# Performance work log

Hardware: AMD Instinct MI355X
Metric: run time of the kernel (lower is better)

## Reference

```python
import jax, jax.numpy as jnp
import numpy as np

D_MODEL, D_K, D_V, H, N, B = 512, 64, 64, 8, 2048, 2


def _xavier(key, shape):
    fan_out, fan_in = shape
    a = jnp.sqrt(6.0 / (fan_in + fan_out))
    return jax.random.uniform(key, shape, jnp.float32, -a, a)


def setup_inputs() -> dict:
    key = jax.random.key(0)
    ks = jax.random.split(key, 12)
    inp = {
        "regions_out": jax.random.normal(ks[0], (B, N, D_MODEL), jnp.float32),
        "grids_out": jax.random.normal(ks[1], (B, N, D_MODEL), jnp.float32),
        "interests": jax.random.normal(ks[2], (B, N, D_MODEL), jnp.float32),
        "attention_mask_regions": jax.random.randint(ks[3], (B, 1, 1, N), 0, 2, jnp.int32),
        "attention_mask_grids": jax.random.randint(ks[4], (B, 1, 1, N), 0, 2, jnp.int32),
        "attention_weights": jax.random.uniform(ks[5], (B, 1, 1, N), jnp.float32),
        # nn.Linear params (weight [out,in], bias [out]); xavier_uniform weights, zero bias
        "Wq": _xavier(ks[6], (H * D_K, D_MODEL)), "bq": jnp.zeros((H * D_K,), jnp.float32),
        "Wk": _xavier(ks[7], (H * D_K, D_MODEL)), "bk": jnp.zeros((H * D_K,), jnp.float32),
        "Wv": _xavier(ks[8], (H * D_V, D_MODEL)), "bv": jnp.zeros((H * D_V,), jnp.float32),
        "Wq12": _xavier(ks[9], (H * D_K, D_MODEL)), "bq12": jnp.zeros((H * D_K,), jnp.float32),
        "Wo1": _xavier(ks[10], (D_MODEL, H * D_V)), "bo1": jnp.zeros((D_MODEL,), jnp.float32),
        "Wo2": _xavier(ks[11], (D_MODEL, H * D_V)), "bo2": jnp.zeros((D_MODEL,), jnp.float32),
    }
    return inp


def _proj(x, W, b, d):
    # x: [b, n, d_model] -> [b, h, n, d]
    b_s, n, _ = x.shape
    y = x @ W.T + b
    return y.reshape(b_s, n, H, d).transpose(0, 2, 1, 3)


def reference(regions_out, grids_out, interests, attention_mask_regions,
              attention_mask_grids, attention_weights,
              Wq, bq, Wk, bk, Wv, bv, Wq12, bq12, Wo1, bo1, Wo2, bo2):
    b_s, nq, _ = interests.shape
    scale = 1.0 / np.sqrt(D_K).astype(np.float32)

    q = _proj(interests, Wq, bq, D_K)          # [b,h,nq,dk]
    q1 = _proj(regions_out, Wq12, bq12, D_K)   # [b,h,nk1,dk]
    q2 = _proj(grids_out, Wq12, bq12, D_K)     # [b,h,nk1,dk]
    k1 = _proj(regions_out, Wk, bk, D_K)       # [b,h,nk1,dk]
    k2 = _proj(grids_out, Wk, bk, D_K)
    v1 = _proj(regions_out, Wv, bv, D_V)
    v2 = _proj(grids_out, Wv, bv, D_V)

    att1 = jnp.einsum("bhqd,bhkd->bhqk", q + q2, k1) * scale
    att2 = jnp.einsum("bhqd,bhkd->bhqk", q + q1, k2) * scale
    att1 = att1 * attention_weights
    att2 = att2 * attention_weights
    att1 = jnp.where(attention_mask_regions.astype(bool), -jnp.inf, att1)
    att2 = jnp.where(attention_mask_grids.astype(bool), -jnp.inf, att2)
    att1 = jax.nn.softmax(att1, axis=-1)
    att2 = jax.nn.softmax(att2, axis=-1)
    # dropout is identity in eval mode

    out1 = jnp.einsum("bhqk,bhkd->bhqd", att1, v1).transpose(0, 2, 1, 3).reshape(b_s, nq, H * D_V)
    out2 = jnp.einsum("bhqk,bhkd->bhqd", att2, v2).transpose(0, 2, 1, 3).reshape(b_s, nq, H * D_V)
    out1 = out1 @ Wo1.T + bo1
    out2 = out2 @ Wo2.T + bo2
    return (out1, out2)
```

## Files before the change

kernel.cpp:

```cpp
#include <hip/hip_runtime.h>
#include <hip/hip_bf16.h>

typedef __attribute__((ext_vector_type(8))) __bf16 bf16x8;
typedef __attribute__((ext_vector_type(4))) float f32x4;
typedef __attribute__((ext_vector_type(4))) int   i32x4;
typedef unsigned short u16;

#define WS_SEG 2097152

static __device__ __forceinline__ u16 f2b(float f) {
  __hip_bfloat16 h = __float2bfloat16(f);
  return __builtin_bit_cast(u16, h);
}
static __device__ __forceinline__ i32x4 cvt8(const float* __restrict__ p) {
  float4 a = *(const float4*)p;
  float4 b = *(const float4*)(p + 4);
  union { i32x4 v; u16 u[8]; } r;
  r.u[0]=f2b(a.x); r.u[1]=f2b(a.y); r.u[2]=f2b(a.z); r.u[3]=f2b(a.w);
  r.u[4]=f2b(b.x); r.u[5]=f2b(b.y); r.u[6]=f2b(b.z); r.u[7]=f2b(b.w);
  return r.v;
}
static __device__ __forceinline__ float fexp2(float x) {
  float r; asm("v_exp_f32 %0, %1" : "=v"(r) : "v"(x)); return r;
}
template<int C>
static __device__ __forceinline__ float dppf(float x) {
  int v = __builtin_amdgcn_update_dpp(__builtin_bit_cast(int, x),
                                      __builtin_bit_cast(int, x), C, 0xF, 0xF, false);
  return __builtin_bit_cast(float, v);
}
static __device__ __forceinline__ float rowsum16(float x) {
  x += dppf<0xB1>(x);
  x += dppf<0x4E>(x);
  x += dppf<0x141>(x);
  x += dppf<0x140>(x);
  return x;
}
static __device__ __forceinline__ void gld16(const u16* gp, u16* lp) {
  __builtin_amdgcn_global_load_lds(
      (const __attribute__((address_space(1))) void*)gp,
      (__attribute__((address_space(3))) void*)lp, 16, 0, 0);
}

__global__ __launch_bounds__(256) void convert_kernel(
    const float* __restrict__ regions, const float* __restrict__ grids,
    const float* __restrict__ interests,
    const float* __restrict__ Wq, const float* __restrict__ Wk,
    const float* __restrict__ Wv, const float* __restrict__ Wq12,
    const float* __restrict__ Wo1, const float* __restrict__ Wo2,
    u16* __restrict__ ws)
{
  const size_t i = (size_t)(blockIdx.x * 256 + threadIdx.x) * 8;
  const float* s; u16* d;
  if (i < 2097152)      { s = regions   + i;           d = ws + 6 * WS_SEG + i; }
  else if (i < 4194304) { s = grids     + (i - 2097152); d = ws + 7 * WS_SEG + (i - 2097152); }
  else if (i < 6291456) { s = interests + (i - 4194304); d = ws + 8 * WS_SEG + (i - 4194304); }
  else {
    const size_t j = i - 6291456;
    d = ws + 9 * WS_SEG + j;
    if (j < 262144)       s = Wq  + j;
    else if (j < 524288)  s = Wk  + (j - 262144);
    else if (j < 786432)  s = Wv  + (j - 524288);
    else if (j < 1048576) s = Wq12+ (j - 786432);
    else if (j < 1310720) s = Wo1 + (j - 1048576);
    else                  s = Wo2 + (j - 1310720);
  }
  *(i32x4*)d = cvt8(s);
}

template<int MT>
__global__ __launch_bounds__(256, 2) void gemm_all(
    const float* __restrict__ aw,
    const float* __restrict__ bq,  const float* __restrict__ bk,
    const float* __restrict__ bv,  const float* __restrict__ bq12,
    const float* __restrict__ bo1, const float* __restrict__ bo2,
    u16* __restrict__ ws, float* __restrict__ out, int phase)
{
  __shared__ u16 As[MT * 64];
  __shared__ u16 Bs[128 * 64];
  constexpr int MFR = MT / 32;

  const u16* regs_bf = ws + 6 * WS_SEG;
  const u16* grid_bf = ws + 7 * WS_SEG;
  const u16* intr_bf = ws + 8 * WS_SEG;
  const u16* Wt      = ws + 9 * WS_SEG;

  const u16 *A1 = nullptr, *A2 = nullptr, *B1 = nullptr, *B2 = nullptr;
  const float *bias1 = nullptr, *bias2 = nullptr;
  u16* dst16 = nullptr;
  float* dst32 = nullptr;
  int KT = 512, epi = 0;
  const int z = blockIdx.z;
  if (phase == 0) {
    if (z == 0)      { A1=intr_bf; A2=grid_bf; B1=Wt; B2=Wt+786432; KT=1024; bias1=bq; bias2=bq12; epi=0; dst16=ws+0*WS_SEG; }
    else if (z == 1) { A1=intr_bf; A2=regs_bf; B1=Wt; B2=Wt+786432; KT=1024; bias1=bq; bias2=bq12; epi=0; dst16=ws+1*WS_SEG; }
    else if (z == 2) { A1=regs_bf; B1=Wt+262144; bias1=bk; epi=1; dst16=ws+2*WS_SEG; }
    else if (z == 3) { A1=grid_bf; B1=Wt+262144; bias1=bk; epi=1; dst16=ws+3*WS_SEG; }
    else if (z == 4) { A1=regs_bf; B1=Wt+524288; bias1=bv; epi=3; dst16=ws+4*WS_SEG; }
    else             { A1=grid_bf; B1=Wt+524288; bias1=bv; epi=3; dst16=ws+5*WS_SEG; }
  } else {
    if (z == 0) { A1=ws+6*WS_SEG; B1=Wt+1048576; bias1=bo1; epi=2; dst32=out; }
    else        { A1=ws+7*WS_SEG; B1=Wt+1310720; bias1=bo2; epi=2; dst32=out + 2097152; }
  }
  const bool swp = (epi == 3);

  const int t = threadIdx.x;
  const int lane = t & 63, w = t >> 6;
  const int l15 = lane & 15, q4 = lane >> 4;
  const int m0 = blockIdx.y * MT, j0 = blockIdx.x * 128;
  const int ro = (w >> 1) * (MT / 2), co = (w & 1) * 64;

  f32x4 acc[MFR][4];
  for (int i = 0; i < MFR; i++)
    for (int j = 0; j < 4; j++) acc[i][j] = (f32x4){0.f, 0.f, 0.f, 0.f};

  for (int k0 = 0; k0 < KT; k0 += 64) {
    const u16* pa; const u16* pb; int kk = k0, ra, rb;
    if (swp)           { pa = B1; pb = A1; ra = j0; rb = m0; }
    else if (kk < 512) { pa = A1; pb = B1; ra = m0; rb = j0; }
    else               { pa = A2; pb = B2; ra = m0; rb = j0; kk -= 512; }
    __syncthreads();
#pragma unroll
    for (int c = 0; c < MFR; c++) {
      const int cidx = w * MFR + c;
      const int row = cidx * 8 + (lane >> 3);
      const int cg = (lane & 7) ^ (row & 7);
      gld16(&pa[(ra + row) * 512 + kk + cg * 8], &As[cidx * 512]);
    }
#pragma unroll
    for (int c = 0; c < 4; c++) {
      const int cidx = w * 4 + c;
      const int row = cidx * 8 + (lane >> 3);
      const int cg = (lane & 7) ^ (row & 7);
      gld16(&pb[(rb + row) * 512 + kk + cg * 8], &Bs[cidx * 512]);
    }
    __syncthreads();
#pragma unroll
    for (int h = 0; h < 2; h++) {
      bf16x8 af[MFR], bfr[4];
#pragma unroll
      for (int i = 0; i < MFR; i++) {
        const int r = ro + i * 16 + l15;
        af[i] = *(const bf16x8*)&As[r * 64 + (((h * 4 + q4) ^ (r & 7)) * 8)];
      }
#pragma unroll
      for (int i = 0; i < 4; i++) {
        const int r = co + i * 16 + l15;
        bfr[i] = *(const bf16x8*)&Bs[r * 64 + (((h * 4 + q4) ^ (r & 7)) * 8)];
      }
#pragma unroll
      for (int mt = 0; mt < MFR; mt++)
#pragma unroll
        for (int nt = 0; nt < 4; nt++)
          acc[mt][nt] = __builtin_amdgcn_mfma_f32_16x16x32_bf16(af[mt], bfr[nt], acc[mt][nt], 0, 0, 0);
    }
  }

  if (epi == 2) {
#pragma unroll
    for (int nt = 0; nt < 4; nt++) {
      const int j = j0 + co + nt * 16 + l15;
      const float bsum = bias1[j];
#pragma unroll
      for (int mt = 0; mt < MFR; mt++)
#pragma unroll
        for (int r = 0; r < 4; r++) {
          const int m = m0 + ro + mt * 16 + q4 * 4 + r;
          dst32[m * 512 + j] = acc[mt][nt][r] + bsum;
        }
    }
    return;
  }

  __syncthreads();
  u16* Es = ((w < 2) ? As : Bs) + (w & 1) * 4096;

  if (epi == 3) {
#pragma unroll
    for (int mt = 0; mt < MFR; mt++)
#pragma unroll
      for (int r = 0; r < 4; r++) {
        const int rr = mt * 16 + q4 * 4 + r;
        const float bias = bias1[j0 + ro + rr];
#pragma unroll
        for (int nt = 0; nt < 4; nt++)
          Es[rr * 64 + (((nt * 2 + (l15 >> 3)) ^ (rr & 7)) * 8) + (l15 & 7)] =
              f2b(acc[mt][nt][r] + bias);
      }
  } else {
    float bsum4[4];
#pragma unroll
    for (int nt = 0; nt < 4; nt++) {
      const int j = j0 + co + nt * 16 + l15;
      bsum4[nt] = bias1[j] + (bias2 ? bias2[j] : 0.f);
    }
#pragma unroll
    for (int mt = 0; mt < MFR; mt++)
#pragma unroll
      for (int r = 0; r < 4; r++) {
        const int rr = mt * 16 + q4 * 4 + r;
        const float awm = (epi == 1) ? 0.18033688f * aw[m0 + ro + rr] : 1.f;
#pragma unroll
        for (int nt = 0; nt < 4; nt++)
          Es[rr * 64 + (((nt * 2 + (l15 >> 3)) ^ (rr & 7)) * 8) + (l15 & 7)] =
              f2b((acc[mt][nt][r] + bsum4[nt]) * awm);
      }
  }
  asm volatile("s_waitcnt lgkmcnt(0)" ::: "memory");

#pragma unroll
  for (int g = 0; g < 8; g++) {
    const int rr2 = g * 8 + (lane >> 3);
    i32x4 val = *(const i32x4*)&Es[rr2 * 64 + (((lane & 7) ^ (rr2 & 7)) * 8)];
    if (epi == 3) {
      const int hd = j0 + ro + rr2;
      const int token0 = m0 + co;
      *(i32x4*)&dst16[((size_t)(token0 >> 11) * 512 + hd) * 2048 + (token0 & 2047) + (lane & 7) * 8] = val;
    } else {
      const int tk = m0 + ro + rr2;
      *(i32x4*)&dst16[(size_t)tk * 512 + j0 + co + (lane & 7) * 8] = val;
    }
  }
}

__global__ __launch_bounds__(256, 2) void attn_kernel(
    const int* __restrict__ mask_r, const int* __restrict__ mask_g,
    u16* __restrict__ ws)
{
  const int qt = blockIdx.x, bh = blockIdx.y, path = blockIdx.z;
  const int b = bh >> 3, h = bh & 7;
  const u16* Q  = (path ? ws + 1 * WS_SEG : ws + 0 * WS_SEG) + (size_t)(b * 2048 + qt * 128) * 512 + h * 64;
  const u16* K  = (path ? ws + 3 * WS_SEG : ws + 2 * WS_SEG) + (size_t)(b * 2048) * 512 + h * 64;
  const u16* Vg = (path ? ws + 5 * WS_SEG : ws + 4 * WS_SEG) + (size_t)(b * 512 + h * 64) * 2048;
  const int* mask = (path ? mask_g : mask_r) + b * 2048;
  u16* O = (path ? ws + 7 * WS_SEG : ws + 6 * WS_SEG) + (size_t)(b * 2048 + qt * 128) * 512 + h * 64;

  __shared__ u16 Ks[64 * 64];
  __shared__ u16 Vs[64 * 64];
  __shared__ u16 Ps[128 * 64];
  __shared__ float Ms[2048];

  const int t = threadIdx.x, lane = t & 63, w = t >> 6;
  const int l15 = lane & 15, q4 = lane >> 4;

  {
    const int4 a = *(const int4*)&mask[t * 8];
    const int4 c = *(const int4*)&mask[t * 8 + 4];
    float4 f1, f2v;
    f1.x = (a.x ? -1e30f : 0.f) - 16.f; f1.y = (a.y ? -1e30f : 0.f) - 16.f;
    f1.z = (a.z ? -1e30f : 0.f) - 16.f; f1.w = (a.w ? -1e30f : 0.f) - 16.f;
    f2v.x = (c.x ? -1e30f : 0.f) - 16.f; f2v.y = (c.y ? -1e30f : 0.f) - 16.f;
    f2v.z = (c.z ? -1e30f : 0.f) - 16.f; f2v.w = (c.w ? -1e30f : 0.f) - 16.f;
    *(float4*)&Ms[t * 8] = f1;
    *(float4*)&Ms[t * 8 + 4] = f2v;
  }

  bf16x8 qf[2][2];
#pragma unroll
  for (int mt = 0; mt < 2; mt++) {
    const int qrow = w * 32 + mt * 16 + l15;
    qf[mt][0] = *(const bf16x8*)&Q[qrow * 512 + q4 * 8];
    qf[mt][1] = *(const bf16x8*)&Q[qrow * 512 + 32 + q4 * 8];
  }

  float l_run[2][4];
  f32x4 o_acc[2][4];
#pragma unroll
  for (int mt = 0; mt < 2; mt++) {
#pragma unroll
    for (int r = 0; r < 4; r++) l_run[mt][r] = 0.f;
#pragma unroll
    for (int d = 0; d < 4; d++) o_acc[mt][d] = (f32x4){0.f, 0.f, 0.f, 0.f};
  }

  for (int kt = 0; kt < 32; kt++) {
    __syncthreads();
#pragma unroll
    for (int c = 0; c < 2; c++) {
      const int cidx = w * 2 + c;
      const int row = cidx * 8 + (lane >> 3);
      const int cg = (lane & 7) ^ (row & 7);
      gld16(&K[(size_t)(kt * 64 + row) * 512 + cg * 8], &Ks[cidx * 512]);
      gld16(&Vg[row * 2048 + kt * 64 + cg * 8], &Vs[cidx * 512]);
    }
    __syncthreads();

    f32x4 s[2][4];
#pragma unroll
    for (int mt = 0; mt < 2; mt++)
#pragma unroll
      for (int nt = 0; nt < 4; nt++) s[mt][nt] = (f32x4){0.f, 0.f, 0.f, 0.f};
#pragma unroll
    for (int nt = 0; nt < 4; nt++)
#pragma unroll
      for (int ss = 0; ss < 2; ss++) {
        const int r = nt * 16 + l15;
        bf16x8 kf = *(const bf16x8*)&Ks[r * 64 + (((ss * 4 + q4) ^ (r & 7)) * 8)];
        s[0][nt] = __builtin_amdgcn_mfma_f32_16x16x32_bf16(qf[0][ss], kf, s[0][nt], 0, 0, 0);
        s[1][nt] = __builtin_amdgcn_mfma_f32_16x16x32_bf16(qf[1][ss], kf, s[1][nt], 0, 0, 0);
      }

#pragma unroll
    for (int nt = 0; nt < 4; nt++) {
      const float bias = Ms[kt * 64 + nt * 16 + l15];
#pragma unroll
      for (int mt = 0; mt < 2; mt++)
#pragma unroll
        for (int r = 0; r < 4; r++) {
          const float p = fexp2(s[mt][nt][r] + bias);
          s[mt][nt][r] = p;
          l_run[mt][r] += p;
        }
    }

#pragma unroll
    for (int mt = 0; mt < 2; mt++)
#pragma unroll
      for (int nt = 0; nt < 4; nt++) {
        const int cg = 2 * nt + (l15 >> 3);
#pragma unroll
        for (int r = 0; r < 4; r++) {
          const int row = w * 32 + mt * 16 + q4 * 4 + r;
          Ps[row * 64 + ((cg ^ (row & 7)) * 8) + (l15 & 7)] = f2b(s[mt][nt][r]);
        }
      }
    asm volatile("s_waitcnt lgkmcnt(0)" ::: "memory");

#pragma unroll
    for (int ss = 0; ss < 2; ss++) {
      bf16x8 pf[2];
#pragma unroll
      for (int mt = 0; mt < 2; mt++) {
        const int row = w * 32 + mt * 16 + l15;
        const int cg = (4 * ss + q4) ^ (row & 7);
        pf[mt] = *(const bf16x8*)&Ps[row * 64 + cg * 8];
      }
#pragma unroll
      for (int dt = 0; dt < 4; dt++) {
        const int r = dt * 16 + l15;
        bf16x8 vf = *(const bf16x8*)&Vs[r * 64 + (((ss * 4 + q4) ^ (r & 7)) * 8)];
        o_acc[0][dt] = __builtin_amdgcn_mfma_f32_16x16x32_bf16(pf[0], vf, o_acc[0][dt], 0, 0, 0);
        o_acc[1][dt] = __builtin_amdgcn_mfma_f32_16x16x32_bf16(pf[1], vf, o_acc[1][dt], 0, 0, 0);
      }
    }
  }

  float inv[2][4];
#pragma unroll
  for (int mt = 0; mt < 2; mt++)
#pragma unroll
    for (int r = 0; r < 4; r++) inv[mt][r] = 1.f / rowsum16(l_run[mt][r]);

#pragma unroll
  for (int mt = 0; mt < 2; mt++)
#pragma unroll
    for (int r = 0; r < 4; r++) {
      const int row = w * 32 + mt * 16 + q4 * 4 + r;
#pragma unroll
      for (int dt = 0; dt < 4; dt++)
        Ps[row * 64 + (((dt * 2 + (l15 >> 3)) ^ (row & 7)) * 8) + (l15 & 7)] =
            f2b(o_acc[mt][dt][r] * inv[mt][r]);
    }
  asm volatile("s_waitcnt lgkmcnt(0)" ::: "memory");
#pragma unroll
  for (int g = 0; g < 4; g++) {
    const int rl = w * 32 + g * 8 + (lane >> 3);
    i32x4 val = *(const i32x4*)&Ps[rl * 64 + (((lane & 7) ^ (rl & 7)) * 8)];
    *(i32x4*)&O[(size_t)rl * 512 + (lane & 7) * 8] = val;
  }
}

extern "C" void kernel_launch(void* const* d_in, const int* in_sizes, int n_in,
                              void* d_out, int out_size, void* d_ws, size_t ws_size,
                              hipStream_t stream) {
  const float* regions   = (const float*)d_in[0];
  const float* grids     = (const float*)d_in[1];
  const float* interests = (const float*)d_in[2];
  const int*   mask_r    = (const int*)d_in[3];
  const int*   mask_g    = (const int*)d_in[4];
  const float* aw        = (const float*)d_in[5];
  const float* Wq  = (const float*)d_in[6];  const float* bq  = (const float*)d_in[7];
  const float* Wk  = (const float*)d_in[8];  const float* bk  = (const float*)d_in[9];
  const float* Wv  = (const float*)d_in[10]; const float* bv  = (const float*)d_in[11];
  const float* Wq12= (const float*)d_in[12]; const float* bq12= (const float*)d_in[13];
  const float* Wo1 = (const float*)d_in[14]; const float* bo1 = (const float*)d_in[15];
  const float* Wo2 = (const float*)d_in[16]; const float* bo2 = (const float*)d_in[17];
  u16*   ws  = (u16*)d_ws;
  float* out = (float*)d_out;

  convert_kernel<<<3840, 256, 0, stream>>>(regions, grids, interests,
      Wq, Wk, Wv, Wq12, Wo1, Wo2, ws);
  gemm_all<128><<<dim3(4, 32, 6), 256, 0, stream>>>(aw, bq, bk, bv, bq12, bo1, bo2,
      ws, out, 0);
  attn_kernel<<<dim3(16, 16, 2), 256, 0, stream>>>(mask_r, mask_g, ws);
  gemm_all<64><<<dim3(4, 64, 2), 256, 0, stream>>>(aw, bq, bk, bv, bq12, bo1, bo2,
      ws, out, 1);
}
```

Before: 203.7 us.

## Double-buffer GEMM and attention LDS tiles and store Q/K head-major

Both the projection GEMM and the attention kernel now keep two LDS buffers and issue the next tile's global-to-LDS loads before computing on the current one. Partial vmcnt waits plus raw barriers replace the pair of __syncthreads per iteration, so memory latency can overlap MFMA work. Q and K projections are now written in a per-(batch, head) contiguous [2048x64] layout, so attention reads them with a 64-element row stride instead of 512. The cost is twice the LDS for the staged tiles, which may lower occupancy, and correctness depends on the hand-counted vmcnt values.

```diff
diff --git a/kernel.cpp b/kernel.cpp
--- a/kernel.cpp
+++ b/kernel.cpp
@@ -7,6 +7,9 @@
 typedef unsigned short u16;
 
 #define WS_SEG 2097152
+
+#define BAR()   asm volatile("s_barrier" ::: "memory")
+#define WAITV0()  asm volatile("s_waitcnt vmcnt(0)" ::: "memory")
 
 static __device__ __forceinline__ u16 f2b(float f) {
   __hip_bfloat16 h = __float2bfloat16(f);
@@ -76,9 +79,9 @@
     const float* __restrict__ bo1, const float* __restrict__ bo2,
     u16* __restrict__ ws, float* __restrict__ out, int phase)
 {
-  __shared__ u16 As[MT * 64];
-  __shared__ u16 Bs[128 * 64];
   constexpr int MFR = MT / 32;
+  __shared__ u16 As[2][MT * 64];
+  __shared__ u16 Bs[2][128 * 64];
 
   const u16* regs_bf = ws + 6 * WS_SEG;
   const u16* grid_bf = ws + 7 * WS_SEG;
@@ -110,43 +113,55 @@
   const int m0 = blockIdx.y * MT, j0 = blockIdx.x * 128;
   const int ro = (w >> 1) * (MT / 2), co = (w & 1) * 64;
 
-  f32x4 acc[MFR][4];
-  for (int i = 0; i < MFR; i++)
-    for (int j = 0; j < 4; j++) acc[i][j] = (f32x4){0.f, 0.f, 0.f, 0.f};
-
-  for (int k0 = 0; k0 < KT; k0 += 64) {
-    const u16* pa; const u16* pb; int kk = k0, ra, rb;
+  auto stageAB = [&](int buf, int k0x) {
+    const u16* pa; const u16* pb; int kk = k0x, ra, rb;
     if (swp)           { pa = B1; pb = A1; ra = j0; rb = m0; }
     else if (kk < 512) { pa = A1; pb = B1; ra = m0; rb = j0; }
     else               { pa = A2; pb = B2; ra = m0; rb = j0; kk -= 512; }
-    __syncthreads();
 #pragma unroll
     for (int c = 0; c < MFR; c++) {
       const int cidx = w * MFR + c;
       const int row = cidx * 8 + (lane >> 3);
       const int cg = (lane & 7) ^ (row & 7);
-      gld16(&pa[(ra + row) * 512 + kk + cg * 8], &As[cidx * 512]);
+      gld16(&pa[(size_t)(ra + row) * 512 + kk + cg * 8], &As[buf][cidx * 512]);
     }
 #pragma unroll
     for (int c = 0; c < 4; c++) {
       const int cidx = w * 4 + c;
       const int row = cidx * 8 + (lane >> 3);
       const int cg = (lane & 7) ^ (row & 7);
-      gld16(&pb[(rb + row) * 512 + kk + cg * 8], &Bs[cidx * 512]);
-    }
-    __syncthreads();
+      gld16(&pb[(size_t)(rb + row) * 512 + kk + cg * 8], &Bs[buf][cidx * 512]);
+    }
+  };
+
+  f32x4 acc[MFR][4];
+  for (int i = 0; i < MFR; i++)
+    for (int j = 0; j < 4; j++) acc[i][j] = (f32x4){0.f, 0.f, 0.f, 0.f};
+
+  stageAB(0, 0);
+  const int NIT = KT / 64;
+  for (int it = 0; it < NIT; it++) {
+    const int cur = it & 1;
+    if (it + 1 < NIT) {
+      stageAB(cur ^ 1, (it + 1) * 64);
+      if (MT == 128) asm volatile("s_waitcnt vmcnt(8)" ::: "memory");
+      else           asm volatile("s_waitcnt vmcnt(6)" ::: "memory");
+    } else {
+      WAITV0();
+    }
+    BAR();
 #pragma unroll
     for (int h = 0; h < 2; h++) {
       bf16x8 af[MFR], bfr[4];
 #pragma unroll
       for (int i = 0; i < MFR; i++) {
         const int r = ro + i * 16 + l15;
-        af[i] = *(const bf16x8*)&As[r * 64 + (((h * 4 + q4) ^ (r & 7)) * 8)];
+        af[i] = *(const bf16x8*)&As[cur][r * 64 + (((h * 4 + q4) ^ (r & 7)) * 8)];
       }
 #pragma unroll
       for (int i = 0; i < 4; i++) {
         const int r = co + i * 16 + l15;
-        bfr[i] = *(const bf16x8*)&Bs[r * 64 + (((h * 4 + q4) ^ (r & 7)) * 8)];
+        bfr[i] = *(const bf16x8*)&Bs[cur][r * 64 + (((h * 4 + q4) ^ (r & 7)) * 8)];
       }
 #pragma unroll
       for (int mt = 0; mt < MFR; mt++)
@@ -154,6 +169,7 @@
         for (int nt = 0; nt < 4; nt++)
           acc[mt][nt] = __builtin_amdgcn_mfma_f32_16x16x32_bf16(af[mt], bfr[nt], acc[mt][nt], 0, 0, 0);
     }
+    BAR();
   }
 
   if (epi == 2) {
@@ -172,8 +188,7 @@
     return;
   }
 
-  __syncthreads();
-  u16* Es = ((w < 2) ? As : Bs) + (w & 1) * 4096;
+  u16* Es = (u16*)As + w * (MT / 2) * 64;
 
   if (epi == 3) {
 #pragma unroll
@@ -209,7 +224,7 @@
   asm volatile("s_waitcnt lgkmcnt(0)" ::: "memory");
 
 #pragma unroll
-  for (int g = 0; g < 8; g++) {
+  for (int g = 0; g < MT / 16; g++) {
     const int rr2 = g * 8 + (lane >> 3);
     i32x4 val = *(const i32x4*)&Es[rr2 * 64 + (((lane & 7) ^ (rr2 & 7)) * 8)];
     if (epi == 3) {
@@ -217,8 +232,10 @@
       const int token0 = m0 + co;
       *(i32x4*)&dst16[((size_t)(token0 >> 11) * 512 + hd) * 2048 + (token0 & 2047) + (lane & 7) * 8] = val;
     } else {
-      const int tk = m0 + ro + rr2;
-      *(i32x4*)&dst16[(size_t)tk * 512 + j0 + co + (lane & 7) * 8] = val;
+      const int token = m0 + ro + rr2;
+      const int bb = token >> 11, nn = token & 2047;
+      const int h = (j0 + co) >> 6;
+      *(i32x4*)&dst16[((size_t)(bb * 8 + h) * 2048 + nn) * 64 + (lane & 7) * 8] = val;
     }
   }
 }
@@ -229,19 +246,30 @@
 {
   const int qt = blockIdx.x, bh = blockIdx.y, path = blockIdx.z;
   const int b = bh >> 3, h = bh & 7;
-  const u16* Q  = (path ? ws + 1 * WS_SEG : ws + 0 * WS_SEG) + (size_t)(b * 2048 + qt * 128) * 512 + h * 64;
-  const u16* K  = (path ? ws + 3 * WS_SEG : ws + 2 * WS_SEG) + (size_t)(b * 2048) * 512 + h * 64;
+  const u16* Q  = (path ? ws + 1 * WS_SEG : ws + 0 * WS_SEG) + (size_t)bh * (2048 * 64) + qt * 128 * 64;
+  const u16* K  = (path ? ws + 3 * WS_SEG : ws + 2 * WS_SEG) + (size_t)bh * (2048 * 64);
   const u16* Vg = (path ? ws + 5 * WS_SEG : ws + 4 * WS_SEG) + (size_t)(b * 512 + h * 64) * 2048;
   const int* mask = (path ? mask_g : mask_r) + b * 2048;
   u16* O = (path ? ws + 7 * WS_SEG : ws + 6 * WS_SEG) + (size_t)(b * 2048 + qt * 128) * 512 + h * 64;
 
-  __shared__ u16 Ks[64 * 64];
-  __shared__ u16 Vs[64 * 64];
+  __shared__ u16 Ks[2][64 * 64];
+  __shared__ u16 Vs[2][64 * 64];
   __shared__ u16 Ps[128 * 64];
   __shared__ float Ms[2048];
 
   const int t = threadIdx.x, lane = t & 63, w = t >> 6;
   const int l15 = lane & 15, q4 = lane >> 4;
+
+  auto stageKV = [&](int buf, int kt) {
+#pragma unroll
+    for (int c = 0; c < 2; c++) {
+      const int cidx = w * 2 + c;
+      const int row = cidx * 8 + (lane >> 3);
+      const int cg = (lane & 7) ^ (row & 7);
+      gld16(&K[(size_t)(kt * 64 + row) * 64 + cg * 8], &Ks[buf][cidx * 512]);
+      gld16(&Vg[(size_t)row * 2048 + kt * 64 + cg * 8], &Vs[buf][cidx * 512]);
+    }
+  };
 
   {
     const int4 a = *(const int4*)&mask[t * 8];
@@ -259,8 +287,8 @@
 #pragma unroll
   for (int mt = 0; mt < 2; mt++) {
     const int qrow = w * 32 + mt * 16 + l15;
-    qf[mt][0] = *(const bf16x8*)&Q[qrow * 512 + q4 * 8];
-    qf[mt][1] = *(const bf16x8*)&Q[qrow * 512 + 32 + q4 * 8];
+    qf[mt][0] = *(const bf16x8*)&Q[qrow * 64 + q4 * 8];
+    qf[mt][1] = *(const bf16x8*)&Q[qrow * 64 + 32 + q4 * 8];
   }
 
   float l_run[2][4];
@@ -273,17 +301,18 @@
     for (int d = 0; d < 4; d++) o_acc[mt][d] = (f32x4){0.f, 0.f, 0.f, 0.f};
   }
 
+  stageKV(0, 0);
+  __syncthreads();
+
   for (int kt = 0; kt < 32; kt++) {
-    __syncthreads();
-#pragma unroll
-    for (int c = 0; c < 2; c++) {
-      const int cidx = w * 2 + c;
-      const int row = cidx * 8 + (lane >> 3);
-      const int cg = (lane & 7) ^ (row & 7);
-      gld16(&K[(size_t)(kt * 64 + row) * 512 + cg * 8], &Ks[cidx * 512]);
-      gld16(&Vg[row * 2048 + kt * 64 + cg * 8], &Vs[cidx * 512]);
-    }
-    __syncthreads();
+    const int cur = kt & 1;
+    if (kt + 1 < 32) {
+      stageKV(cur ^ 1, kt + 1);
+      asm volatile("s_waitcnt vmcnt(4)" ::: "memory");
+    } else {
+      WAITV0();
+    }
+    BAR();
 
     f32x4 s[2][4];
 #pragma unroll
@@ -295,7 +324,7 @@
 #pragma unroll
       for (int ss = 0; ss < 2; ss++) {
         const int r = nt * 16 + l15;
-        bf16x8 kf = *(const bf16x8*)&Ks[r * 64 + (((ss * 4 + q4) ^ (r & 7)) * 8)];
+        bf16x8 kf = *(const bf16x8*)&Ks[cur][r * 64 + (((ss * 4 + q4) ^ (r & 7)) * 8)];
         s[0][nt] = __builtin_amdgcn_mfma_f32_16x16x32_bf16(qf[0][ss], kf, s[0][nt], 0, 0, 0);
         s[1][nt] = __builtin_amdgcn_mfma_f32_16x16x32_bf16(qf[1][ss], kf, s[1][nt], 0, 0, 0);
       }
@@ -338,11 +367,12 @@
 #pragma unroll
       for (int dt = 0; dt < 4; dt++) {
         const int r = dt * 16 + l15;
-        bf16x8 vf = *(const bf16x8*)&Vs[r * 64 + (((ss * 4 + q4) ^ (r & 7)) * 8)];
+        bf16x8 vf = *(const bf16x8*)&Vs[cur][r * 64 + (((ss * 4 + q4) ^ (r & 7)) * 8)];
         o_acc[0][dt] = __builtin_amdgcn_mfma_f32_16x16x32_bf16(pf[0], vf, o_acc[0][dt], 0, 0, 0);
         o_acc[1][dt] = __builtin_amdgcn_mfma_f32_16x16x32_bf16(pf[1], vf, o_acc[1][dt], 0, 0, 0);
       }
     }
+    BAR();
   }
 
   float inv[2][4];
```

Measured after the change: 211.2 us. 3.7% more time.

## Store Q/K head-major, shrink GEMM and attention tiles, split V projection launch

Applied to the files above, without the earlier changes.

Q and K projections are now written in a per-head [b,h,n,64] layout so the attention kernel reads contiguous 64-wide rows instead of 512-strided ones. GEMM tiles shrink to 128x64 or 64x64 with launch bounds raised to 4 waves per SIMD, and the V projection moves into its own launch with swapped operand roles. The attention kernel drops to 64 query rows per block, giving twice the blocks with less register and LDS pressure. In exchange, K/V tiles are reloaded by more blocks and there is one extra kernel launch.

```diff
diff --git a/kernel.cpp b/kernel.cpp
--- a/kernel.cpp
+++ b/kernel.cpp
@@ -68,17 +68,19 @@
   *(i32x4*)d = cvt8(s);
 }
 
-template<int MT>
-__global__ __launch_bounds__(256, 2) void gemm_all(
+template<int MT, int NT>
+__global__ __launch_bounds__(256, 4) void gemm_all(
     const float* __restrict__ aw,
     const float* __restrict__ bq,  const float* __restrict__ bk,
     const float* __restrict__ bv,  const float* __restrict__ bq12,
     const float* __restrict__ bo1, const float* __restrict__ bo2,
     u16* __restrict__ ws, float* __restrict__ out, int phase)
 {
-  __shared__ u16 As[MT * 64];
-  __shared__ u16 Bs[128 * 64];
   constexpr int MFR = MT / 32;
+  constexpr int NFR = NT / 32;
+  __shared__ u16 SM[(MT + NT) * 64];
+  u16* As = SM;
+  u16* Bs = SM + MT * 64;
 
   const u16* regs_bf = ws + 6 * WS_SEG;
   const u16* grid_bf = ws + 7 * WS_SEG;
@@ -95,70 +97,69 @@
     if (z == 0)      { A1=intr_bf; A2=grid_bf; B1=Wt; B2=Wt+786432; KT=1024; bias1=bq; bias2=bq12; epi=0; dst16=ws+0*WS_SEG; }
     else if (z == 1) { A1=intr_bf; A2=regs_bf; B1=Wt; B2=Wt+786432; KT=1024; bias1=bq; bias2=bq12; epi=0; dst16=ws+1*WS_SEG; }
     else if (z == 2) { A1=regs_bf; B1=Wt+262144; bias1=bk; epi=1; dst16=ws+2*WS_SEG; }
-    else if (z == 3) { A1=grid_bf; B1=Wt+262144; bias1=bk; epi=1; dst16=ws+3*WS_SEG; }
-    else if (z == 4) { A1=regs_bf; B1=Wt+524288; bias1=bv; epi=3; dst16=ws+4*WS_SEG; }
-    else             { A1=grid_bf; B1=Wt+524288; bias1=bv; epi=3; dst16=ws+5*WS_SEG; }
+    else             { A1=grid_bf; B1=Wt+262144; bias1=bk; epi=1; dst16=ws+3*WS_SEG; }
+  } else if (phase == 2) {
+    if (z == 0) { A1=Wt+524288; B1=regs_bf; bias1=bv; epi=3; dst16=ws+4*WS_SEG; }
+    else        { A1=Wt+524288; B1=grid_bf; bias1=bv; epi=3; dst16=ws+5*WS_SEG; }
   } else {
     if (z == 0) { A1=ws+6*WS_SEG; B1=Wt+1048576; bias1=bo1; epi=2; dst32=out; }
     else        { A1=ws+7*WS_SEG; B1=Wt+1310720; bias1=bo2; epi=2; dst32=out + 2097152; }
   }
-  const bool swp = (epi == 3);
 
   const int t = threadIdx.x;
   const int lane = t & 63, w = t >> 6;
   const int l15 = lane & 15, q4 = lane >> 4;
-  const int m0 = blockIdx.y * MT, j0 = blockIdx.x * 128;
-  const int ro = (w >> 1) * (MT / 2), co = (w & 1) * 64;
-
-  f32x4 acc[MFR][4];
+  const int m0 = (phase == 2 ? blockIdx.x : blockIdx.y) * MT;
+  const int j0 = (phase == 2 ? blockIdx.y : blockIdx.x) * NT;
+  const int ro = (w >> 1) * (MT / 2), co = (w & 1) * (NT / 2);
+
+  f32x4 acc[MFR][NFR];
   for (int i = 0; i < MFR; i++)
-    for (int j = 0; j < 4; j++) acc[i][j] = (f32x4){0.f, 0.f, 0.f, 0.f};
+    for (int j = 0; j < NFR; j++) acc[i][j] = (f32x4){0.f, 0.f, 0.f, 0.f};
 
   for (int k0 = 0; k0 < KT; k0 += 64) {
-    const u16* pa; const u16* pb; int kk = k0, ra, rb;
-    if (swp)           { pa = B1; pb = A1; ra = j0; rb = m0; }
-    else if (kk < 512) { pa = A1; pb = B1; ra = m0; rb = j0; }
-    else               { pa = A2; pb = B2; ra = m0; rb = j0; kk -= 512; }
+    const u16* pa = A1; const u16* pb = B1; int kk = k0;
+    if (kk >= 512) { pa = A2; pb = B2; kk -= 512; }
     __syncthreads();
 #pragma unroll
     for (int c = 0; c < MFR; c++) {
       const int cidx = w * MFR + c;
       const int row = cidx * 8 + (lane >> 3);
       const int cg = (lane & 7) ^ (row & 7);
-      gld16(&pa[(ra + row) * 512 + kk + cg * 8], &As[cidx * 512]);
-    }
-#pragma unroll
-    for (int c = 0; c < 4; c++) {
-      const int cidx = w * 4 + c;
+      gld16(&pa[(size_t)(m0 + row) * 512 + kk + cg * 8], &As[cidx * 512]);
+    }
+#pragma unroll
+    for (int c = 0; c < NFR; c++) {
+      const int cidx = w * NFR + c;
       const int row = cidx * 8 + (lane >> 3);
       const int cg = (lane & 7) ^ (row & 7);
-      gld16(&pb[(rb + row) * 512 + kk + cg * 8], &Bs[cidx * 512]);
+      gld16(&pb[(size_t)(j0 + row) * 512 + kk + cg * 8], &Bs[cidx * 512]);
     }
     __syncthreads();
 #pragma unroll
     for (int h = 0; h < 2; h++) {
-      bf16x8 af[MFR], bfr[4];
+      bf16x8 af[MFR], bfr[NFR];
 #pragma unroll
       for (int i = 0; i < MFR; i++) {
         const int r = ro + i * 16 + l15;
         af[i] = *(const bf16x8*)&As[r * 64 + (((h * 4 + q4) ^ (r & 7)) * 8)];
       }
 #pragma unroll
-      for (int i = 0; i < 4; i++) {
+      for (int i = 0; i < NFR; i++) {
         const int r = co + i * 16 + l15;
         bfr[i] = *(const bf16x8*)&Bs[r * 64 + (((h * 4 + q4) ^ (r & 7)) * 8)];
       }
 #pragma unroll
       for (int mt = 0; mt < MFR; mt++)
 #pragma unroll
-        for (int nt = 0; nt < 4; nt++)
+        for (int nt = 0; nt < NFR; nt++)
           acc[mt][nt] = __builtin_amdgcn_mfma_f32_16x16x32_bf16(af[mt], bfr[nt], acc[mt][nt], 0, 0, 0);
     }
   }
 
   if (epi == 2) {
 #pragma unroll
-    for (int nt = 0; nt < 4; nt++) {
+    for (int nt = 0; nt < NFR; nt++) {
       const int j = j0 + co + nt * 16 + l15;
       const float bsum = bias1[j];
 #pragma unroll
@@ -173,7 +174,7 @@
   }
 
   __syncthreads();
-  u16* Es = ((w < 2) ? As : Bs) + (w & 1) * 4096;
+  u16* Es = SM + w * (MT / 2) * 40;
 
   if (epi == 3) {
 #pragma unroll
@@ -181,16 +182,15 @@
 #pragma unroll
       for (int r = 0; r < 4; r++) {
         const int rr = mt * 16 + q4 * 4 + r;
-        const float bias = bias1[j0 + ro + rr];
-#pragma unroll
-        for (int nt = 0; nt < 4; nt++)
-          Es[rr * 64 + (((nt * 2 + (l15 >> 3)) ^ (rr & 7)) * 8) + (l15 & 7)] =
-              f2b(acc[mt][nt][r] + bias);
+        const float bias = bias1[m0 + ro + rr];
+#pragma unroll
+        for (int nt = 0; nt < NFR; nt++)
+          Es[rr * 40 + nt * 16 + l15] = f2b(acc[mt][nt][r] + bias);
       }
   } else {
-    float bsum4[4];
-#pragma unroll
-    for (int nt = 0; nt < 4; nt++) {
+    float bsum4[NFR];
+#pragma unroll
+    for (int nt = 0; nt < NFR; nt++) {
       const int j = j0 + co + nt * 16 + l15;
       bsum4[nt] = bias1[j] + (bias2 ? bias2[j] : 0.f);
     }
@@ -201,43 +201,45 @@
         const int rr = mt * 16 + q4 * 4 + r;
         const float awm = (epi == 1) ? 0.18033688f * aw[m0 + ro + rr] : 1.f;
 #pragma unroll
-        for (int nt = 0; nt < 4; nt++)
-          Es[rr * 64 + (((nt * 2 + (l15 >> 3)) ^ (rr & 7)) * 8) + (l15 & 7)] =
-              f2b((acc[mt][nt][r] + bsum4[nt]) * awm);
+        for (int nt = 0; nt < NFR; nt++)
+          Es[rr * 40 + nt * 16 + l15] = f2b((acc[mt][nt][r] + bsum4[nt]) * awm);
       }
   }
   asm volatile("s_waitcnt lgkmcnt(0)" ::: "memory");
 
 #pragma unroll
-  for (int g = 0; g < 8; g++) {
-    const int rr2 = g * 8 + (lane >> 3);
-    i32x4 val = *(const i32x4*)&Es[rr2 * 64 + (((lane & 7) ^ (rr2 & 7)) * 8)];
+  for (int g = 0; g < MT / 32; g++) {
+    const int rr2 = g * 16 + (lane >> 2);
+    i32x4 val = *(const i32x4*)&Es[rr2 * 40 + (lane & 3) * 8];
     if (epi == 3) {
-      const int hd = j0 + ro + rr2;
-      const int token0 = m0 + co;
-      *(i32x4*)&dst16[((size_t)(token0 >> 11) * 512 + hd) * 2048 + (token0 & 2047) + (lane & 7) * 8] = val;
+      const int hd = m0 + ro + rr2;
+      const int token0 = j0 + co;
+      *(i32x4*)&dst16[((size_t)(token0 >> 11) * 512 + hd) * 2048 + (token0 & 2047) + (lane & 3) * 8] = val;
     } else {
-      const int tk = m0 + ro + rr2;
-      *(i32x4*)&dst16[(size_t)tk * 512 + j0 + co + (lane & 7) * 8] = val;
-    }
-  }
-}
-
-__global__ __launch_bounds__(256, 2) void attn_kernel(
+      const int token = m0 + ro + rr2;
+      const int bb = token >> 11, nn = token & 2047;
+      const int hd0 = j0 + co;
+      const int hh = hd0 >> 6, db = hd0 & 63;
+      *(i32x4*)&dst16[((size_t)(bb * 8 + hh) * 2048 + nn) * 64 + db + (lane & 3) * 8] = val;
+    }
+  }
+}
+
+__global__ __launch_bounds__(256, 4) void attn_kernel(
     const int* __restrict__ mask_r, const int* __restrict__ mask_g,
     u16* __restrict__ ws)
 {
   const int qt = blockIdx.x, bh = blockIdx.y, path = blockIdx.z;
   const int b = bh >> 3, h = bh & 7;
-  const u16* Q  = (path ? ws + 1 * WS_SEG : ws + 0 * WS_SEG) + (size_t)(b * 2048 + qt * 128) * 512 + h * 64;
-  const u16* K  = (path ? ws + 3 * WS_SEG : ws + 2 * WS_SEG) + (size_t)(b * 2048) * 512 + h * 64;
+  const u16* Q  = (path ? ws + 1 * WS_SEG : ws + 0 * WS_SEG) + (size_t)bh * (2048 * 64) + qt * 64 * 64;
+  const u16* K  = (path ? ws + 3 * WS_SEG : ws + 2 * WS_SEG) + (size_t)bh * (2048 * 64);
   const u16* Vg = (path ? ws + 5 * WS_SEG : ws + 4 * WS_SEG) + (size_t)(b * 512 + h * 64) * 2048;
   const int* mask = (path ? mask_g : mask_r) + b * 2048;
-  u16* O = (path ? ws + 7 * WS_SEG : ws + 6 * WS_SEG) + (size_t)(b * 2048 + qt * 128) * 512 + h * 64;
+  u16* O = (path ? ws + 7 * WS_SEG : ws + 6 * WS_SEG) + (size_t)(b * 2048 + qt * 64) * 512 + h * 64;
 
   __shared__ u16 Ks[64 * 64];
   __shared__ u16 Vs[64 * 64];
-  __shared__ u16 Ps[128 * 64];
+  __shared__ u16 Ps[64 * 64];
   __shared__ float Ms[2048];
 
   const int t = threadIdx.x, lane = t & 63, w = t >> 6;
@@ -255,23 +257,19 @@
     *(float4*)&Ms[t * 8 + 4] = f2v;
   }
 
-  bf16x8 qf[2][2];
-#pragma unroll
-  for (int mt = 0; mt < 2; mt++) {
-    const int qrow = w * 32 + mt * 16 + l15;
-    qf[mt][0] = *(const bf16x8*)&Q[qrow * 512 + q4 * 8];
-    qf[mt][1] = *(const bf16x8*)&Q[qrow * 512 + 32 + q4 * 8];
-  }
-
-  float l_run[2][4];
-  f32x4 o_acc[2][4];
-#pragma unroll
-  for (int mt = 0; mt < 2; mt++) {
-#pragma unroll
-    for (int r = 0; r < 4; r++) l_run[mt][r] = 0.f;
-#pragma unroll
-    for (int d = 0; d < 4; d++) o_acc[mt][d] = (f32x4){0.f, 0.f, 0.f, 0.f};
-  }
+  bf16x8 qf[2];
+  {
+    const int qrow = w * 16 + l15;
+    qf[0] = *(const bf16x8*)&Q[qrow * 64 + q4 * 8];
+    qf[1] = *(const bf16x8*)&Q[qrow * 64 + 32 + q4 * 8];
+  }
+
+  float l_run[4];
+  f32x4 o_acc[4];
+#pragma unroll
+  for (int r = 0; r < 4; r++) l_run[r] = 0.f;
+#pragma unroll
+  for (int d = 0; d < 4; d++) o_acc[d] = (f32x4){0.f, 0.f, 0.f, 0.f};
 
   for (int kt = 0; kt < 32; kt++) {
     __syncthreads();
@@ -280,91 +278,75 @@
       const int cidx = w * 2 + c;
       const int row = cidx * 8 + (lane >> 3);
       const int cg = (lane & 7) ^ (row & 7);
-      gld16(&K[(size_t)(kt * 64 + row) * 512 + cg * 8], &Ks[cidx * 512]);
-      gld16(&Vg[row * 2048 + kt * 64 + cg * 8], &Vs[cidx * 512]);
+      gld16(&K[(size_t)(kt * 64 + row) * 64 + cg * 8], &Ks[cidx * 512]);
+      gld16(&Vg[(size_t)row * 2048 + kt * 64 + cg * 8], &Vs[cidx * 512]);
     }
     __syncthreads();
 
-    f32x4 s[2][4];
-#pragma unroll
-    for (int mt = 0; mt < 2; mt++)
-#pragma unroll
-      for (int nt = 0; nt < 4; nt++) s[mt][nt] = (f32x4){0.f, 0.f, 0.f, 0.f};
+    f32x4 s[4];
+#pragma unroll
+    for (int nt = 0; nt < 4; nt++) s[nt] = (f32x4){0.f, 0.f, 0.f, 0.f};
 #pragma unroll
     for (int nt = 0; nt < 4; nt++)
 #pragma unroll
       for (int ss = 0; ss < 2; ss++) {
         const int r = nt * 16 + l15;
         bf16x8 kf = *(const bf16x8*)&Ks[r * 64 + (((ss * 4 + q4) ^ (r & 7)) * 8)];
-        s[0][nt] = __builtin_amdgcn_mfma_f32_16x16x32_bf16(qf[0][ss], kf, s[0][nt], 0, 0, 0);
-        s[1][nt] = __builtin_amdgcn_mfma_f32_16x16x32_bf16(qf[1][ss], kf, s[1][nt], 0, 0, 0);
+        s[nt] = __builtin_amdgcn_mfma_f32_16x16x32_bf16(qf[ss], kf, s[nt], 0, 0, 0);
       }
 
 #pragma unroll
     for (int nt = 0; nt < 4; nt++) {
       const float bias = Ms[kt * 64 + nt * 16 + l15];
 #pragma unroll
-      for (int mt = 0; mt < 2; mt++)
-#pragma unroll
-        for (int r = 0; r < 4; r++) {
-          const float p = fexp2(s[mt][nt][r] + bias);
-          s[mt][nt][r] = p;
-          l_run[mt][r] += p;
-        }
-    }
-
-#pragma unroll
-    for (int mt = 0; mt < 2; mt++)
-#pragma unroll
-      for (int nt = 0; nt < 4; nt++) {
-        const int cg = 2 * nt + (l15 >> 3);
-#pragma unroll
-        for (int r = 0; r < 4; r++) {
-          const int row = w * 32 + mt * 16 + q4 * 4 + r;
-          Ps[row * 64 + ((cg ^ (row & 7)) * 8) + (l15 & 7)] = f2b(s[mt][nt][r]);
-        }
-      }
+      for (int r = 0; r < 4; r++) {
+        const float p = fexp2(s[nt][r] + bias);
+        s[nt][r] = p;
+        l_run[r] += p;
+      }
+    }
+
+#pragma unroll
+    for (int nt = 0; nt < 4; nt++) {
+      const int cg = 2 * nt + (l15 >> 3);
+#pragma unroll
+      for (int r = 0; r < 4; r++) {
+        const int row = w * 16 + q4 * 4 + r;
+        Ps[row * 64 + ((cg ^ (row & 7)) * 8) + (l15 & 7)] = f2b(s[nt][r]);
+      }
+    }
     asm volatile("s_waitcnt lgkmcnt(0)" ::: "memory");
 
 #pragma unroll
     for (int ss = 0; ss < 2; ss++) {
-      bf16x8 pf[2];
-#pragma unroll
-      for (int mt = 0; mt < 2; mt++) {
-        const int row = w * 32 + mt * 16 + l15;
-        const int cg = (4 * ss + q4) ^ (row & 7);
-        pf[mt] = *(const bf16x8*)&Ps[row * 64 + cg * 8];
-      }
+      const int row = w * 16 + l15;
+      const int cg = (4 * ss + q4) ^ (row & 7);
+      bf16x8 pf = *(const bf16x8*)&Ps[row * 64 + cg * 8];
 #pragma unroll
       for (int dt = 0; dt < 4; dt++) {
         const int r = dt * 16 + l15;
         bf16x8 vf = *(const bf16x8*)&Vs[r * 64 + (((ss * 4 + q4) ^ (r & 7)) * 8)];
-        o_acc[0][dt] = __builtin_amdgcn_mfma_f32_16x16x32_bf16(pf[0], vf, o_acc[0][dt], 0, 0, 0);
-        o_acc[1][dt] = __builtin_amdgcn_mfma_f32_16x16x32_bf16(pf[1], vf, o_acc[1][dt], 0, 0, 0);
-      }
-    }
-  }
-
-  float inv[2][4];
-#pragma unroll
-  for (int mt = 0; mt < 2; mt++)
-#pragma unroll
-    for (int r = 0; r < 4; r++) inv[mt][r] = 1.f / rowsum16(l_run[mt][r]);
-
-#pragma unroll
-  for (int mt = 0; mt < 2; mt++)
-#pragma unroll
-    for (int r = 0; r < 4; r++) {
-      const int row = w * 32 + mt * 16 + q4 * 4 + r;
-#pragma unroll
-      for (int dt = 0; dt < 4; dt++)
-        Ps[row * 64 + (((dt * 2 + (l15 >> 3)) ^ (row & 7)) * 8) + (l15 & 7)] =
-            f2b(o_acc[mt][dt][r] * inv[mt][r]);
-    }
+        o_acc[dt] = __builtin_amdgcn_mfma_f32_16x16x32_bf16(pf, vf, o_acc[dt], 0, 0, 0);
+      }
+    }
+  }
+
+  float inv[4];
+#pragma unroll
+  for (int r = 0; r < 4; r++) inv[r] = 1.f / rowsum16(l_run[r]);
+
+#pragma unroll
+  for (int r = 0; r < 4; r++) {
+    const int row = w * 16 + q4 * 4 + r;
+#pragma unroll
+    for (int dt = 0; dt < 4; dt++)
+      Ps[row * 64 + (((dt * 2 + (l15 >> 3)) ^ (row & 7)) * 8) + (l15 & 7)] =
+          f2b(o_acc[dt][r] * inv[r]);
+  }
   asm volatile("s_waitcnt lgkmcnt(0)" ::: "memory");
 #pragma unroll
-  for (int g = 0; g < 4; g++) {
-    const int rl = w * 32 + g * 8 + (lane >> 3);
+  for (int g = 0; g < 2; g++) {
+    const int rl = w * 16 + g * 8 + (lane >> 3);
     i32x4 val = *(const i32x4*)&Ps[rl * 64 + (((lane & 7) ^ (rl & 7)) * 8)];
     *(i32x4*)&O[(size_t)rl * 512 + (lane & 7) * 8] = val;
   }
@@ -390,9 +372,11 @@
 
   convert_kernel<<<3840, 256, 0, stream>>>(regions, grids, interests,
       Wq, Wk, Wv, Wq12, Wo1, Wo2, ws);
-  gemm_all<128><<<dim3(4, 32, 6), 256, 0, stream>>>(aw, bq, bk, bv, bq12, bo1, bo2,
-      ws, out, 0);
-  attn_kernel<<<dim3(16, 16, 2), 256, 0, stream>>>(mask_r, mask_g, ws);
-  gemm_all<64><<<dim3(4, 64, 2), 256, 0, stream>>>(aw, bq, bk, bv, bq12, bo1, bo2,
-      ws, out, 1);
-}
+  gemm_all<128, 64><<<dim3(8, 32, 4), 256, 0, stream>>>(aw, bq, bk, bv, bq12,
+      bo1, bo2, ws, out, 0);
+  gemm_all<128, 64><<<dim3(4, 64, 2), 256, 0, stream>>>(aw, bq, bk, bv, bq12,
+      bo1, bo2, ws, out, 2);
+  attn_kernel<<<dim3(32, 16, 2), 256, 0, stream>>>(mask_r, mask_g, ws);
+  gemm_all<64, 64><<<dim3(8, 64, 2), 256, 0, stream>>>(aw, bq, bk, bv, bq12,
+      bo1, bo2, ws, out, 1);
+}
```

Measured after the change: 218.7 us. +7.4%, slower.

## Store Q/K head-major, linearize grid ordering, write attention output directly

Applied to the files above, without the earlier changes.

The Q and K projection epilogues now write head-major [b,h,n,64] tiles, so attention blocks read contiguous 128-byte rows instead of rows strided by 512 elements. The 3D grids become 1D with explicit index decoding, which changes block scheduling order: M tiles now vary fastest in the GEMMs, and heads/paths vary fastest in attention. The attention epilogue drops the LDS staging round-trip and stores bf16 scalars straight to global memory, which risks less-coalesced writes. LDS in the GEMM is merged into one array so the epilogue scratch region is addressed uniformly.

```diff
diff --git a/kernel.cpp b/kernel.cpp
--- a/kernel.cpp
+++ b/kernel.cpp
@@ -68,7 +68,7 @@
   *(i32x4*)d = cvt8(s);
 }
 
-template<int MT>
+template<int MT, int NM>
 __global__ __launch_bounds__(256, 2) void gemm_all(
     const float* __restrict__ aw,
     const float* __restrict__ bq,  const float* __restrict__ bk,
@@ -76,21 +76,27 @@
     const float* __restrict__ bo1, const float* __restrict__ bo2,
     u16* __restrict__ ws, float* __restrict__ out, int phase)
 {
-  __shared__ u16 As[MT * 64];
-  __shared__ u16 Bs[128 * 64];
   constexpr int MFR = MT / 32;
+  __shared__ u16 SM[(MT + 128) * 64];
+  u16* As = SM;
+  u16* Bs = SM + MT * 64;
 
   const u16* regs_bf = ws + 6 * WS_SEG;
   const u16* grid_bf = ws + 7 * WS_SEG;
   const u16* intr_bf = ws + 8 * WS_SEG;
   const u16* Wt      = ws + 9 * WS_SEG;
+
+  const int id = blockIdx.x;
+  const int m_idx = id % NM;
+  const int rest  = id / NM;
+  const int j_idx = rest & 3;
+  const int z     = rest >> 2;
 
   const u16 *A1 = nullptr, *A2 = nullptr, *B1 = nullptr, *B2 = nullptr;
   const float *bias1 = nullptr, *bias2 = nullptr;
   u16* dst16 = nullptr;
   float* dst32 = nullptr;
   int KT = 512, epi = 0;
-  const int z = blockIdx.z;
   if (phase == 0) {
     if (z == 0)      { A1=intr_bf; A2=grid_bf; B1=Wt; B2=Wt+786432; KT=1024; bias1=bq; bias2=bq12; epi=0; dst16=ws+0*WS_SEG; }
     else if (z == 1) { A1=intr_bf; A2=regs_bf; B1=Wt; B2=Wt+786432; KT=1024; bias1=bq; bias2=bq12; epi=0; dst16=ws+1*WS_SEG; }
@@ -107,7 +113,7 @@
   const int t = threadIdx.x;
   const int lane = t & 63, w = t >> 6;
   const int l15 = lane & 15, q4 = lane >> 4;
-  const int m0 = blockIdx.y * MT, j0 = blockIdx.x * 128;
+  const int m0 = m_idx * MT, j0 = j_idx * 128;
   const int ro = (w >> 1) * (MT / 2), co = (w & 1) * 64;
 
   f32x4 acc[MFR][4];
@@ -125,14 +131,14 @@
       const int cidx = w * MFR + c;
       const int row = cidx * 8 + (lane >> 3);
       const int cg = (lane & 7) ^ (row & 7);
-      gld16(&pa[(ra + row) * 512 + kk + cg * 8], &As[cidx * 512]);
+      gld16(&pa[(size_t)(ra + row) * 512 + kk + cg * 8], &As[cidx * 512]);
     }
 #pragma unroll
     for (int c = 0; c < 4; c++) {
       const int cidx = w * 4 + c;
       const int row = cidx * 8 + (lane >> 3);
       const int cg = (lane & 7) ^ (row & 7);
-      gld16(&pb[(rb + row) * 512 + kk + cg * 8], &Bs[cidx * 512]);
+      gld16(&pb[(size_t)(rb + row) * 512 + kk + cg * 8], &Bs[cidx * 512]);
     }
     __syncthreads();
 #pragma unroll
@@ -173,7 +179,7 @@
   }
 
   __syncthreads();
-  u16* Es = ((w < 2) ? As : Bs) + (w & 1) * 4096;
+  u16* Es = SM + w * (MT / 2) * 64;
 
   if (epi == 3) {
 #pragma unroll
@@ -209,7 +215,7 @@
   asm volatile("s_waitcnt lgkmcnt(0)" ::: "memory");
 
 #pragma unroll
-  for (int g = 0; g < 8; g++) {
+  for (int g = 0; g < MT / 16; g++) {
     const int rr2 = g * 8 + (lane >> 3);
     i32x4 val = *(const i32x4*)&Es[rr2 * 64 + (((lane & 7) ^ (rr2 & 7)) * 8)];
     if (epi == 3) {
@@ -217,8 +223,10 @@
       const int token0 = m0 + co;
       *(i32x4*)&dst16[((size_t)(token0 >> 11) * 512 + hd) * 2048 + (token0 & 2047) + (lane & 7) * 8] = val;
     } else {
-      const int tk = m0 + ro + rr2;
-      *(i32x4*)&dst16[(size_t)tk * 512 + j0 + co + (lane & 7) * 8] = val;
+      const int token = m0 + ro + rr2;
+      const int bb = token >> 11, nn = token & 2047;
+      const int h = (j0 + co) >> 6;
+      *(i32x4*)&dst16[((size_t)(bb * 8 + h) * 2048 + nn) * 64 + (lane & 7) * 8] = val;
     }
   }
 }
@@ -227,10 +235,13 @@
     const int* __restrict__ mask_r, const int* __restrict__ mask_g,
     u16* __restrict__ ws)
 {
-  const int qt = blockIdx.x, bh = blockIdx.y, path = blockIdx.z;
+  const int id = blockIdx.x;
+  const int bhf = id & 31;
+  const int qt = id >> 5;
+  const int path = bhf >> 4, bh = bhf & 15;
   const int b = bh >> 3, h = bh & 7;
-  const u16* Q  = (path ? ws + 1 * WS_SEG : ws + 0 * WS_SEG) + (size_t)(b * 2048 + qt * 128) * 512 + h * 64;
-  const u16* K  = (path ? ws + 3 * WS_SEG : ws + 2 * WS_SEG) + (size_t)(b * 2048) * 512 + h * 64;
+  const u16* Q  = (path ? ws + 1 * WS_SEG : ws + 0 * WS_SEG) + (size_t)bh * (2048 * 64) + qt * 128 * 64;
+  const u16* K  = (path ? ws + 3 * WS_SEG : ws + 2 * WS_SEG) + (size_t)bh * (2048 * 64);
   const u16* Vg = (path ? ws + 5 * WS_SEG : ws + 4 * WS_SEG) + (size_t)(b * 512 + h * 64) * 2048;
   const int* mask = (path ? mask_g : mask_r) + b * 2048;
   u16* O = (path ? ws + 7 * WS_SEG : ws + 6 * WS_SEG) + (size_t)(b * 2048 + qt * 128) * 512 + h * 64;
@@ -259,8 +270,8 @@
 #pragma unroll
   for (int mt = 0; mt < 2; mt++) {
     const int qrow = w * 32 + mt * 16 + l15;
-    qf[mt][0] = *(const bf16x8*)&Q[qrow * 512 + q4 * 8];
-    qf[mt][1] = *(const bf16x8*)&Q[qrow * 512 + 32 + q4 * 8];
+    qf[mt][0] = *(const bf16x8*)&Q[qrow * 64 + q4 * 8];
+    qf[mt][1] = *(const bf16x8*)&Q[qrow * 64 + 32 + q4 * 8];
   }
 
   float l_run[2][4];
@@ -280,8 +291,8 @@
       const int cidx = w * 2 + c;
       const int row = cidx * 8 + (lane >> 3);
       const int cg = (lane & 7) ^ (row & 7);
-      gld16(&K[(size_t)(kt * 64 + row) * 512 + cg * 8], &Ks[cidx * 512]);
-      gld16(&Vg[row * 2048 + kt * 64 + cg * 8], &Vs[cidx * 512]);
+      gld16(&K[(size_t)(kt * 64 + row) * 64 + cg * 8], &Ks[cidx * 512]);
+      gld16(&Vg[(size_t)row * 2048 + kt * 64 + cg * 8], &Vs[cidx * 512]);
     }
     __syncthreads();
 
@@ -345,29 +356,16 @@
     }
   }
 
-  float inv[2][4];
 #pragma unroll
   for (int mt = 0; mt < 2; mt++)
 #pragma unroll
-    for (int r = 0; r < 4; r++) inv[mt][r] = 1.f / rowsum16(l_run[mt][r]);
-
-#pragma unroll
-  for (int mt = 0; mt < 2; mt++)
-#pragma unroll
     for (int r = 0; r < 4; r++) {
-      const int row = w * 32 + mt * 16 + q4 * 4 + r;
-#pragma unroll
-      for (int dt = 0; dt < 4; dt++)
-        Ps[row * 64 + (((dt * 2 + (l15 >> 3)) ^ (row & 7)) * 8) + (l15 & 7)] =
-            f2b(o_acc[mt][dt][r] * inv[mt][r]);
-    }
-  asm volatile("s_waitcnt lgkmcnt(0)" ::: "memory");
-#pragma unroll
-  for (int g = 0; g < 4; g++) {
-    const int rl = w * 32 + g * 8 + (lane >> 3);
-    i32x4 val = *(const i32x4*)&Ps[rl * 64 + (((lane & 7) ^ (rl & 7)) * 8)];
-    *(i32x4*)&O[(size_t)rl * 512 + (lane & 7) * 8] = val;
-  }
+      const float inv = 1.f / rowsum16(l_run[mt][r]);
+#pragma unroll
+      for (int dt = 0; dt < 4; dt++) {
+        O[(w * 32 + mt * 16 + q4 * 4 + r) * 512 + dt * 16 + l15] = f2b(o_acc[mt][dt][r] * inv);
+      }
+    }
 }
 
 extern "C" void kernel_launch(void* const* d_in, const int* in_sizes, int n_in,
@@ -390,9 +388,9 @@
 
   convert_kernel<<<3840, 256, 0, stream>>>(regions, grids, interests,
       Wq, Wk, Wv, Wq12, Wo1, Wo2, ws);
-  gemm_all<128><<<dim3(4, 32, 6), 256, 0, stream>>>(aw, bq, bk, bv, bq12, bo1, bo2,
+  gemm_all<128, 32><<<768, 256, 0, stream>>>(aw, bq, bk, bv, bq12, bo1, bo2,
       ws, out, 0);
-  attn_kernel<<<dim3(16, 16, 2), 256, 0, stream>>>(mask_r, mask_g, ws);
-  gemm_all<64><<<dim3(4, 64, 2), 256, 0, stream>>>(aw, bq, bk, bv, bq12, bo1, bo2,
+  attn_kernel<<<512, 256, 0, stream>>>(mask_r, mask_g, ws);
+  gemm_all<64, 64><<<512, 256, 0, stream>>>(aw, bq, bk, bv, bq12, bo1, bo2,
       ws, out, 1);
 }
```

Measured after the change: 194.5 us. -4.5%, faster.
